# Optimization experiments

Hardware: AMD Instinct MI355X
Metric: run time of the kernel (lower is better)

The kernel has to match this reference:

```python
import jax, jax.numpy as jnp
import numpy as np

B, S, D = 16, 1024, 64
BASE, SCALE = 10000.0, 1.0


def setup_inputs() -> dict:
    key = jax.random.key(0)
    # geospatial coordinates in [0, 1)
    spa_feat = jax.random.uniform(key, (B, S, 2), dtype=jnp.float32)
    return {"spa_feat": spa_feat}


def reference(spa_feat):
    d = D
    q = d // 4  # number of frequency bands per coordinate axis
    inv_freq = 1.0 / (BASE ** (jnp.arange(q, dtype=jnp.float32) / q))  # [q]
    xy = spa_feat * SCALE                                # [B,S,2]
    freq = xy[..., :, None] * inv_freq                   # [B,S,2,q]
    freq_x, freq_y = freq[..., 0, :], freq[..., 1, :]    # [B,S,q] each
    sin_emb = jnp.concatenate([jnp.sin(freq_x), jnp.sin(freq_y)], axis=-1)  # [B,S,d/2]
    cos_emb = jnp.concatenate([jnp.cos(freq_x), jnp.cos(freq_y)], axis=-1)  # [B,S,d/2]
    b, s, h = sin_emb.shape  # h = d//2 number of 2x2 blocks
    r = 2 * jnp.arange(h)    # top-left row/col index of each 2x2 block
    # Block-diagonal rotation matrix: block i = [[cos_i, -sin_i], [sin_i, cos_i]]
    R = jnp.zeros((b, s, d, d), dtype=sin_emb.dtype)
    R = (R.at[:, :, r, r].set(cos_emb)
           .at[:, :, r, r + 1].set(-sin_emb)
           .at[:, :, r + 1, r].set(sin_emb)
           .at[:, :, r + 1, r + 1].set(cos_emb))
    return R
```

## Files before the change

### kernel.cpp

```cpp
#include <hip/hip_runtime.h>


#define NBS 16384

__global__ __launch_bounds__(256) void rope2d_kernel(
    const float* __restrict__ spa,
    float* __restrict__ out)
{
    const int bs = blockIdx.x;
    const int t  = threadIdx.x;

    const float xu = spa[bs * 2 + 0];
    const float yu = spa[bs * 2 + 1];

    const int  cg   = t & 15;
    const int  wq   = t >> 6;
    const int  diff = cg - wq;
    const bool has  = (diff >= 0) && ((diff & 3) == 0);
    const int  ks   = diff >> 2;

    float4* __restrict__ outv = (float4*)out + (size_t)bs * 1024;
    const float4 z4 = make_float4(0.f, 0.f, 0.f, 0.f);

    #pragma unroll
    for (int k = 0; k < 4; ++k) {
        if (!(has && k == ks))
            outv[t + k * 256] = z4;
    }

    if (has) {
        const int row = (t >> 4) + (ks << 4);
        const int h   = row >> 1;
        const float xy   = (h & 16) ? yu : xu;
        const float invf = exp2f(-(float)(h & 15) * 0.83048202372184059f);
        const float a = xy * invf;
        const float s = sinf(a);
        const float c = cosf(a);
        float e0, e1;
        if (row & 1) { e0 = s; e1 = c; }
        else         { e0 = c; e1 = -s; }
        float4 v;
        if (row & 2) v = make_float4(0.f, 0.f, e0, e1);
        else         v = make_float4(e0, e1, 0.f, 0.f);
        outv[t + ks * 256] = v;
    }
}

extern "C" void kernel_launch(void* const* d_in, const int* in_sizes, int n_in,
                              void* d_out, int out_size, void* d_ws, size_t ws_size,
                              hipStream_t stream) {
    const float* spa = (const float*)d_in[0];
    float* out = (float*)d_out;
    rope2d_kernel<<<NBS, 256, 0, stream>>>(spa, out);
}
```

Baseline: 258.0 us.

## Process eight positions per block with shared-memory sin/cos table

Each block now handles eight (b,s) positions instead of one. All 256 threads first compute the 8x32 sin/cos values once into shared memory, then loop over the positions and write the zero-padded float4 rows. This removes the redundant per-thread transcendental work and cuts the block count eightfold, at the cost of a __syncthreads and shared-memory reads. The kernel is dominated by writing 256 MB of output, so the gain is likely small.

```diff
diff --git a/kernel.cpp b/kernel.cpp
--- a/kernel.cpp
+++ b/kernel.cpp
@@ -1,48 +1,59 @@
 #include <hip/hip_runtime.h>
 
 
-#define NBS 16384
+#define NBS  16384
+#define BSPB 8
+#define NBLK (NBS / BSPB)
 
 __global__ __launch_bounds__(256) void rope2d_kernel(
     const float* __restrict__ spa,
     float* __restrict__ out)
 {
-    const int bs = blockIdx.x;
-    const int t  = threadIdx.x;
+    const int t   = threadIdx.x;
+    const int bs0 = blockIdx.x * BSPB;
 
-    const float xu = spa[bs * 2 + 0];
-    const float yu = spa[bs * 2 + 1];
+    __shared__ float ssin[BSPB * 32];
+    __shared__ float scos[BSPB * 32];
 
-    const int  cg   = t & 15;
-    const int  wq   = t >> 6;
-    const int  diff = cg - wq;
+    {
+        const int m = t >> 5;
+        const int h = t & 31;
+        const float xy   = spa[(bs0 + m) * 2 + (h >> 4)];
+        const float invf = exp2f(-(float)(h & 15) * 0.83048202372184059f);
+        const float a    = xy * invf;
+        ssin[t] = sinf(a);
+        scos[t] = cosf(a);
+    }
+    __syncthreads();
+
+    const int cg    = t & 15;
+    const int rbase = t >> 4;
+    const int diff  = cg - (rbase >> 2);
     const bool has  = (diff >= 0) && ((diff & 3) == 0);
-    const int  ks   = diff >> 2;
+    const int ks    = diff >> 2;
+    const int rows  = rbase + (ks << 4);
+    const int hs    = (rows >> 1) & 31;
+    const int odd   = rows & 1;
+    const int hi    = rows & 2;
 
-    float4* __restrict__ outv = (float4*)out + (size_t)bs * 1024;
+    float4* __restrict__ outv = (float4*)out + (size_t)bs0 * 1024 + t;
     const float4 z4 = make_float4(0.f, 0.f, 0.f, 0.f);
 
     #pragma unroll
-    for (int k = 0; k < 4; ++k) {
-        if (!(has && k == ks))
-            outv[t + k * 256] = z4;
-    }
-
-    if (has) {
-        const int row = (t >> 4) + (ks << 4);
-        const int h   = row >> 1;
-        const float xy   = (h & 16) ? yu : xu;
-        const float invf = exp2f(-(float)(h & 15) * 0.83048202372184059f);
-        const float a = xy * invf;
-        const float s = sinf(a);
-        const float c = cosf(a);
-        float e0, e1;
-        if (row & 1) { e0 = s; e1 = c; }
-        else         { e0 = c; e1 = -s; }
-        float4 v;
-        if (row & 2) v = make_float4(0.f, 0.f, e0, e1);
-        else         v = make_float4(e0, e1, 0.f, 0.f);
-        outv[t + ks * 256] = v;
+    for (int m = 0; m < BSPB; ++m) {
+        float4 vs = z4;
+        if (has) {
+            const float s  = ssin[(m << 5) + hs];
+            const float c  = scos[(m << 5) + hs];
+            const float e0 = odd ? s :  c;
+            const float e1 = odd ? c : -s;
+            if (hi) { vs.z = e0; vs.w = e1; }
+            else    { vs.x = e0; vs.y = e1; }
+        }
+        #pragma unroll
+        for (int k = 0; k < 4; ++k) {
+            outv[m * 1024 + k * 256] = (k == ks) ? vs : z4;
+        }
     }
 }
 
@@ -51,5 +62,5 @@
                               hipStream_t stream) {
     const float* spa = (const float*)d_in[0];
     float* out = (float*)d_out;
-    rope2d_kernel<<<NBS, 256, 0, stream>>>(spa, out);
+    rope2d_kernel<<<NBLK, 256, 0, stream>>>(spa, out);
 }
```

New measurement: 302.9 us. +17.4%, slower.
